# Kernel optimization log

Measured on AMD Instinct MI355X. Metric: run time of the kernel, lower is better.

The kernel has to match this reference:

```python
import jax, jax.numpy as jnp
import numpy as np

Q_EPS = 1e-12  # scale clamp used in from_float


def _quantize_rows(w):
    # per-row symmetric int8 quantization: scale = absmax/127, clamp 1e-12
    scales = jnp.clip(jnp.max(jnp.abs(w), axis=1) / 127.0, Q_EPS, None)  # [rows]
    w_i8 = jnp.clip(jnp.round(w / scales[:, None]), -128.0, 127.0)       # int values, fp32 carrier
    return w_i8, scales


def setup_inputs() -> dict:
    key = jax.random.key(0)
    k1, k2, k3 = jax.random.split(key, 3)
    B, S, K, N = 2, 4096, 4096, 4096
    x = jax.random.normal(k1, (B, S, K), dtype=jnp.float32)
    weight_fp = jax.random.normal(k2, (N, K), dtype=jnp.float32) * 0.02
    bias = jax.random.normal(k3, (N,), dtype=jnp.float32) * 0.01
    return {"x": x, "weight_fp": weight_fp, "bias": bias}


def reference(x, weight_fp, bias):
    orig_dtype = x.dtype
    # weight quantization (from_float): per-output-channel scales
    w_i8, w_scales = _quantize_rows(weight_fp)          # [N,K], [N]
    # per-token dynamic activation quantization
    x_shape = x.shape
    x_flat = x.reshape(-1, x_shape[-1])                 # [M,K]
    x_i8, x_scales = _quantize_rows(x_flat)             # [M,K], [M]
    # int8 GEMM accumulated exactly (values fit fp32), fused dequant
    acc = jnp.matmul(x_i8, w_i8.T)                      # [M,N] integer-valued
    out = acc * x_scales[:, None] * w_scales[None, :]
    out = out.astype(jnp.bfloat16)                      # kernel outputs bf16
    out = out.reshape(*x_shape[:-1], w_i8.shape[0])
    out = out + bias.astype(out.dtype)
    return out.astype(orig_dtype)
```

## Files before the change

kernel.cpp:

```cpp
#include <hip/hip_runtime.h>
#include <hip/hip_bf16.h>
#include <stdint.h>


using i32x4  = __attribute__((ext_vector_type(4))) int;
using i32x16 = __attribute__((ext_vector_type(16))) int;

#define BM 256
#define BN 256
#define BKB 128

__global__ __launch_bounds__(256) void quant_rows_wave(
    const float* __restrict__ w_in, const float* __restrict__ x_in,
    int8_t* __restrict__ w_q, int8_t* __restrict__ x_q,
    float* __restrict__ w_s, float* __restrict__ x_s,
    int nw, int nrows, int K)
{
    const int wave_id = (int)((blockIdx.x * (unsigned)blockDim.x + threadIdx.x) >> 6);
    if (wave_id >= nrows) return;
    const int lane = threadIdx.x & 63;

    const bool is_w = (wave_id < nw);
    const int row = is_w ? wave_id : (wave_id - nw);
    const float* r = (is_w ? w_in : x_in) + (size_t)row * K;
    int8_t* qout   = (is_w ? w_q : x_q) + (size_t)row * K;
    float* scales  = is_w ? w_s : x_s;

    float4 v[16];
#pragma unroll
    for (int i = 0; i < 16; ++i)
        v[i] = *(const float4*)(r + i * 256 + lane * 4);

    float amax = 0.f;
#pragma unroll
    for (int i = 0; i < 16; ++i) {
        amax = fmaxf(amax, fmaxf(fmaxf(fabsf(v[i].x), fabsf(v[i].y)),
                                 fmaxf(fabsf(v[i].z), fabsf(v[i].w))));
    }

#pragma unroll
    for (int off = 32; off >= 1; off >>= 1)
        amax = fmaxf(amax, __shfl_xor(amax, off));

    const float scale = fmaxf(amax / 127.0f, 1e-12f);
    if (lane == 0) scales[row] = scale;
    const float inv = 1.0f / scale;

#pragma unroll
    for (int i = 0; i < 16; ++i) {
        float q0 = fminf(fmaxf(rintf(v[i].x * inv), -128.f), 127.f);
        float q1 = fminf(fmaxf(rintf(v[i].y * inv), -128.f), 127.f);
        float q2 = fminf(fmaxf(rintf(v[i].z * inv), -128.f), 127.f);
        float q3 = fminf(fmaxf(rintf(v[i].w * inv), -128.f), 127.f);
        union { signed char c[4]; int i32; } u;
        u.c[0] = (signed char)(int)q0;
        u.c[1] = (signed char)(int)q1;
        u.c[2] = (signed char)(int)q2;
        u.c[3] = (signed char)(int)q3;
        *(int*)(qout + i * 256 + lane * 4) = u.i32;
    }
}

__global__ __launch_bounds__(512, 2) void gemm_i8_256(
    const int8_t* __restrict__ A,
    const int8_t* __restrict__ B,
    const float*  __restrict__ xs,
    const float*  __restrict__ ws,
    const float*  __restrict__ bias,
    float*        __restrict__ out,
    int M, int N, int K)
{
    __shared__ int8_t sA[2][BM * BKB];
    __shared__ int8_t sB[2][BN * BKB];

    const int tid   = threadIdx.x;
    const int wave  = tid >> 6;
    const int lane  = tid & 63;
    const int l31   = lane & 31;
    const int lhalf = lane >> 5;
    const int rot   = l31 & 7;

    const int bm = blockIdx.y * BM;
    const int bn = blockIdx.x * BN;
    const int wm = (wave >> 2) * 128;
    const int wn = (wave & 3) * 64;

    i32x16 acc[4][2];
#pragma unroll
    for (int q = 0; q < 4; ++q)
#pragma unroll
        for (int n = 0; n < 2; ++n)
#pragma unroll
            for (int r = 0; r < 16; ++r) acc[q][n][r] = 0;

    const int srow = tid >> 3;
    const int soff = (((tid & 7) ^ ((tid >> 3) & 7)) << 4);
    const int8_t* aS = A + (size_t)(bm + srow) * K + soff;
    const int8_t* bS = B + (size_t)(bn + srow) * K + soff;
    const size_t rstep = (size_t)64 * K;

    const int NT = K / BKB;

#define STAGE4(SRC, DST)                                                     \
    {                                                                        \
        _Pragma("unroll")                                                    \
        for (int l = 0; l < 4; ++l)                                          \
            __builtin_amdgcn_global_load_lds(                                \
                (const __attribute__((address_space(1))) void*)((SRC) + l * rstep), \
                (__attribute__((address_space(3))) void*)((DST) + l * 8192 + tid * 16), \
                16, 0, 0);                                                   \
    }

    STAGE4(aS, &sA[0][0]);
    STAGE4(bS, &sB[0][0]);
    asm volatile("s_waitcnt vmcnt(0)" ::: "memory");
    __builtin_amdgcn_s_barrier();
    asm volatile("" ::: "memory");

    for (int t = 0; t < NT; ++t) {
        const int cur = t & 1;
        const int8_t* cA = &sA[cur][0];
        const int8_t* cB = &sB[cur][0];
        int8_t* nA = &sA[cur ^ 1][0];
        int8_t* nB = &sB[cur ^ 1][0];
        const size_t knext = (size_t)(t + 1) * BKB;
        const bool pf = (t + 1 < NT);

        i32x4 bf[2][4];
#pragma unroll
        for (int n = 0; n < 2; ++n)
#pragma unroll
            for (int ks = 0; ks < 4; ++ks) {
                const int row = wn + n * 32 + l31;
                bf[n][ks] = *(const i32x4*)(cB + row * BKB +
                                            ((((ks << 1) | lhalf) ^ rot) << 4));
            }

#pragma unroll
        for (int q = 0; q < 4; ++q) {
            i32x4 af[4];
#pragma unroll
            for (int ks = 0; ks < 4; ++ks) {
                const int row = wm + q * 32 + l31;
                af[ks] = *(const i32x4*)(cA + row * BKB +
                                         ((((ks << 1) | lhalf) ^ rot) << 4));
            }

            if (q == 0 && pf) STAGE4(aS + knext, nA);
            if (q == 1 && pf) STAGE4(bS + knext, nB);

#pragma unroll
            for (int n = 0; n < 2; ++n)
#pragma unroll
                for (int ks = 0; ks < 4; ++ks)
                    acc[q][n] = __builtin_amdgcn_mfma_i32_32x32x32_i8(
                        af[ks], bf[n][ks], acc[q][n], 0, 0, 0);
        }

        asm volatile("s_waitcnt vmcnt(0)" ::: "memory");
        __builtin_amdgcn_s_barrier();
        asm volatile("" ::: "memory");
    }
#undef STAGE4

#pragma unroll
    for (int n = 0; n < 2; ++n) {
        const int col = bn + wn + n * 32 + l31;
        const float wsv = ws[col];
        const float bsv = __bfloat162float(__float2bfloat16(bias[col]));
#pragma unroll
        for (int q = 0; q < 4; ++q) {
            const int rowbase = bm + wm + q * 32 + 4 * lhalf;
#pragma unroll
            for (int r = 0; r < 16; ++r) {
                const int row = rowbase + (r & 3) + 8 * (r >> 2);
                const float v = (float)acc[q][n][r] * xs[row] * wsv;
                const float vb = __bfloat162float(__float2bfloat16(v));
                const float res = __bfloat162float(__float2bfloat16(vb + bsv));
                out[(size_t)row * N + col] = res;
            }
        }
    }
}

extern "C" void kernel_launch(void* const* d_in, const int* in_sizes, int n_in,
                              void* d_out, int out_size, void* d_ws, size_t ws_size,
                              hipStream_t stream)
{
    const float* x    = (const float*)d_in[0];
    const float* wfp  = (const float*)d_in[1];
    const float* bias = (const float*)d_in[2];
    float* out = (float*)d_out;

    const int N = in_sizes[2];
    const int K = in_sizes[1] / N;
    const int M = in_sizes[0] / K;

    int8_t* w_i8 = (int8_t*)d_ws;
    int8_t* x_i8 = w_i8 + (size_t)N * K;
    float* w_scales = (float*)(x_i8 + (size_t)M * K);
    float* x_scales = w_scales + N;

    const int nrows = N + M;
    const int nblocks = (nrows + 3) / 4;
    quant_rows_wave<<<nblocks, 256, 0, stream>>>(wfp, x, w_i8, x_i8,
                                                 w_scales, x_scales,
                                                 N, nrows, K);

    dim3 grid(N / BN, M / BM);
    gemm_i8_256<<<grid, 512, 0, stream>>>(x_i8, w_i8, x_scales, w_scales,
                                          bias, out, M, N, K);
}
```

Measured before the change: 432.9 us.

## Deepen GEMM LDS pipeline to four buffers with prefetch three tiles ahead

Halves the K-tile to 64 bytes and keeps four LDS buffers per operand, issuing global-to-LDS loads three iterations ahead. Partial vmcnt waits replace the full drain each iteration, so more loads can be in flight while MFMAs run. Swizzle offsets are redone for the narrower tile and LDS addresses are precomputed once. In exchange there are twice as many barriers per K, the same LDS footprint, and the tail of the loop needs careful wait counts.

```diff
diff --git a/kernel.cpp b/kernel.cpp
--- a/kernel.cpp
+++ b/kernel.cpp
@@ -8,7 +8,8 @@
 
 #define BM 256
 #define BN 256
-#define BKB 128
+#define BKB 64
+#define NBUF 4
 
 __global__ __launch_bounds__(256) void quant_rows_wave(
     const float* __restrict__ w_in, const float* __restrict__ x_in,
@@ -61,7 +62,7 @@
     }
 }
 
-__global__ __launch_bounds__(512, 2) void gemm_i8_256(
+__global__ __launch_bounds__(512, 2) void gemm_i8_p3(
     const int8_t* __restrict__ A,
     const int8_t* __restrict__ B,
     const float*  __restrict__ xs,
@@ -70,15 +71,15 @@
     float*        __restrict__ out,
     int M, int N, int K)
 {
-    __shared__ int8_t sA[2][BM * BKB];
-    __shared__ int8_t sB[2][BN * BKB];
+    __shared__ int8_t sA[NBUF][BM * BKB];
+    __shared__ int8_t sB[NBUF][BN * BKB];
 
     const int tid   = threadIdx.x;
     const int wave  = tid >> 6;
     const int lane  = tid & 63;
     const int l31   = lane & 31;
     const int lhalf = lane >> 5;
-    const int rot   = l31 & 7;
+    const int rot4  = (l31 + (l31 >> 2)) & 3;
 
     const int bm = blockIdx.y * BM;
     const int bn = blockIdx.x * BN;
@@ -93,75 +94,91 @@
 #pragma unroll
             for (int r = 0; r < 16; ++r) acc[q][n][r] = 0;
 
-    const int srow = tid >> 3;
-    const int soff = (((tid & 7) ^ ((tid >> 3) & 7)) << 4);
+    int aoff[4][2], boff[2][2];
+#pragma unroll
+    for (int q = 0; q < 4; ++q)
+#pragma unroll
+        for (int ks = 0; ks < 2; ++ks)
+            aoff[q][ks] = (wm + q * 32 + l31) * BKB +
+                          (((((ks << 1) | lhalf) + rot4) & 3) << 4);
+#pragma unroll
+    for (int n = 0; n < 2; ++n)
+#pragma unroll
+        for (int ks = 0; ks < 2; ++ks)
+            boff[n][ks] = (wn + n * 32 + l31) * BKB +
+                          (((((ks << 1) | lhalf) + rot4) & 3) << 4);
+
+    const int srow = tid >> 2;
+    const int soff = ((((tid & 3) - (tid >> 2) - (tid >> 4)) & 3) << 4);
     const int8_t* aS = A + (size_t)(bm + srow) * K + soff;
     const int8_t* bS = B + (size_t)(bn + srow) * K + soff;
-    const size_t rstep = (size_t)64 * K;
+    const size_t rstep = (size_t)128 * K;
 
     const int NT = K / BKB;
 
-#define STAGE4(SRC, DST)                                                     \
+#define STAGE(SRC, DSTBASE)                                                  \
     {                                                                        \
         _Pragma("unroll")                                                    \
-        for (int l = 0; l < 4; ++l)                                          \
+        for (int l = 0; l < 2; ++l)                                          \
             __builtin_amdgcn_global_load_lds(                                \
                 (const __attribute__((address_space(1))) void*)((SRC) + l * rstep), \
-                (__attribute__((address_space(3))) void*)((DST) + l * 8192 + tid * 16), \
+                (__attribute__((address_space(3))) void*)((DSTBASE) + l * 8192 + tid * 16), \
                 16, 0, 0);                                                   \
     }
 
-    STAGE4(aS, &sA[0][0]);
-    STAGE4(bS, &sB[0][0]);
-    asm volatile("s_waitcnt vmcnt(0)" ::: "memory");
+#pragma unroll
+    for (int p = 0; p < 3; ++p) {
+        STAGE(aS + p * BKB, &sA[p][0]);
+        STAGE(bS + p * BKB, &sB[p][0]);
+    }
+    asm volatile("s_waitcnt vmcnt(8)" ::: "memory");
     __builtin_amdgcn_s_barrier();
     asm volatile("" ::: "memory");
 
     for (int t = 0; t < NT; ++t) {
-        const int cur = t & 1;
-        const int8_t* cA = &sA[cur][0];
-        const int8_t* cB = &sB[cur][0];
-        int8_t* nA = &sA[cur ^ 1][0];
-        int8_t* nB = &sB[cur ^ 1][0];
-        const size_t knext = (size_t)(t + 1) * BKB;
-        const bool pf = (t + 1 < NT);
-
-        i32x4 bf[2][4];
+        const int8_t* cA = &sA[t & 3][0];
+        const int8_t* cB = &sB[t & 3][0];
+        const bool pf = (t + 3 < NT);
+        const size_t knext = (size_t)(t + 3) * BKB;
+        int8_t* nA = &sA[(t + 3) & 3][0];
+        int8_t* nB = &sB[(t + 3) & 3][0];
+
+        i32x4 bf[2][2];
 #pragma unroll
         for (int n = 0; n < 2; ++n)
 #pragma unroll
-            for (int ks = 0; ks < 4; ++ks) {
-                const int row = wn + n * 32 + l31;
-                bf[n][ks] = *(const i32x4*)(cB + row * BKB +
-                                            ((((ks << 1) | lhalf) ^ rot) << 4));
-            }
+            for (int ks = 0; ks < 2; ++ks)
+                bf[n][ks] = *(const i32x4*)(cB + boff[n][ks]);
 
 #pragma unroll
         for (int q = 0; q < 4; ++q) {
-            i32x4 af[4];
-#pragma unroll
-            for (int ks = 0; ks < 4; ++ks) {
-                const int row = wm + q * 32 + l31;
-                af[ks] = *(const i32x4*)(cA + row * BKB +
-                                         ((((ks << 1) | lhalf) ^ rot) << 4));
-            }
-
-            if (q == 0 && pf) STAGE4(aS + knext, nA);
-            if (q == 1 && pf) STAGE4(bS + knext, nB);
+            i32x4 af[2];
+#pragma unroll
+            for (int ks = 0; ks < 2; ++ks)
+                af[ks] = *(const i32x4*)(cA + aoff[q][ks]);
+
+            if (q == 0 && pf) STAGE(aS + knext, nA);
+            if (q == 1 && pf) STAGE(bS + knext, nB);
 
 #pragma unroll
             for (int n = 0; n < 2; ++n)
 #pragma unroll
-                for (int ks = 0; ks < 4; ++ks)
+                for (int ks = 0; ks < 2; ++ks)
                     acc[q][n] = __builtin_amdgcn_mfma_i32_32x32x32_i8(
                         af[ks], bf[n][ks], acc[q][n], 0, 0, 0);
         }
 
-        asm volatile("s_waitcnt vmcnt(0)" ::: "memory");
+        if (t + 3 < NT) {
+            asm volatile("s_waitcnt vmcnt(8)" ::: "memory");
+        } else if (t + 3 == NT) {
+            asm volatile("s_waitcnt vmcnt(4)" ::: "memory");
+        } else if (t + 2 == NT) {
+            asm volatile("s_waitcnt vmcnt(0)" ::: "memory");
+        }
         __builtin_amdgcn_s_barrier();
         asm volatile("" ::: "memory");
     }
-#undef STAGE4
+#undef STAGE
 
 #pragma unroll
     for (int n = 0; n < 2; ++n) {
@@ -208,6 +225,6 @@
                                                  N, nrows, K);
 
     dim3 grid(N / BN, M / BM);
-    gemm_i8_256<<<grid, 512, 0, stream>>>(x_i8, w_i8, x_scales, w_scales,
-                                          bias, out, M, N, K);
+    gemm_i8_p3<<<grid, 512, 0, stream>>>(x_i8, w_i8, x_scales, w_scales,
+                                         bias, out, M, N, K);
 }
```

New measurement: 444.7 us. 1.03x slower.
